# Kernel tuning notes

Measured on AMD Instinct MI355X. Metric: run time of the kernel, lower is better.

Reference implementation:

```python
import jax, jax.numpy as jnp
import numpy as np

S = 2048          # sequence length
E = 1024          # embedding_size
C = 16            # channels
ED = E // C       # per-channel dim e
VOCAB = 32000
EPS = 1e-8        # torch cosine_similarity eps


def setup_inputs() -> dict:
    key = jax.random.key(0)
    k0, k1, k2, k3, k4 = jax.random.split(key, 5)
    seqs = jax.random.randint(k0, (S,), 0, VOCAB - 1)  # avoid padding idx VOCAB-1
    emb = jax.random.uniform(k1, (VOCAB, E), minval=-0.05, maxval=0.05, dtype=jnp.float32)
    Wl = jax.random.normal(k2, (C, ED), dtype=jnp.float32) * 0.1
    Wr = jax.random.normal(k3, (C, ED), dtype=jnp.float32) * 0.1
    b = jax.random.normal(k4, (C, ED), dtype=jnp.float32) * 0.01
    return {"seqs": seqs, "emb": emb, "Wl": Wl, "Wr": Wr, "b": b}


def reference(seqs, emb, Wl, Wr, b):
    # Banyan.compose_words: greedy cosine-similarity adjacent-pair merge.
    # Fixed-size buffer + validity mask replaces torch's shrinking tensor so the
    # S-1 sequential merge steps run under a single lax.scan.
    x0 = emb[seqs]                      # [S, E]
    valid0 = jnp.ones((S,), dtype=bool)
    ar = jnp.arange(S)

    def comp(l, r):
        # channel-wise composition: view(2, c, e) -> parent [E]
        lc = l.reshape(C, ED)
        rc = r.reshape(C, ED)
        return jnp.tanh(lc * Wl + rc * Wr + b).reshape(E)

    def step(carry, _):
        x, valid = carry
        # next valid index for each position (suffix-min trick)
        idxs = jnp.where(valid, ar, S)
        nxt = jnp.flip(jax.lax.cummin(jnp.flip(jnp.append(idxs[1:], S))))
        pair_ok = valid & (nxt < S)
        xn = x[jnp.minimum(nxt, S - 1)]  # [S, E] right neighbor
        num = jnp.sum(x * xn, axis=-1)
        den = jnp.maximum(jnp.linalg.norm(x, axis=-1), EPS) * \
              jnp.maximum(jnp.linalg.norm(xn, axis=-1), EPS)
        cos = jnp.where(pair_ok, num / den, -jnp.inf)
        i = jnp.argmax(cos)              # left index of best adjacent pair
        j = nxt[i]                       # right index
        parent = comp(x[i], x[j])
        x = x.at[j].set(parent)          # parent overwrites right slot
        valid = valid.at[i].set(False)   # left slot removed
        return (x, valid), None

    (x, valid), _ = jax.lax.scan(step, (x0, valid0), None, length=S - 1)
    # exactly one valid slot remains -> root embedding [E]
    return jnp.sum(x * valid[:, None].astype(x.dtype), axis=0)
```

## Files before the change

kernel.cpp:

```cpp
#include <hip/hip_runtime.h>
#include <math.h>

#define SS 2048
#define EE 1024
#define EPSD 1e-8
#define EPSF 1e-8f
#define NTH 256
#define NW  4
#define NG  32
#define GS  64

#define DPP_XOR1 0xB1
#define DPP_XOR2 0x4E
#define DPP_HMIR 0x141
#define DPP_MIR  0x140

using f4 = float __attribute__((ext_vector_type(4)));
using f2 = float __attribute__((ext_vector_type(2)));

__device__ __forceinline__ void bar_lds() {
  asm volatile("s_waitcnt lgkmcnt(0)" ::: "memory");
  __builtin_amdgcn_s_barrier();
  __builtin_amdgcn_sched_barrier(0);
}

template <int CTRL>
__device__ __forceinline__ float mov_dpp_f32(float v) {
  union { float f; int i; } a; a.f = v;
  const int n = __builtin_amdgcn_mov_dpp(a.i, CTRL, 0xF, 0xF, true);
  union { int i; float f; } r; r.i = n;
  return r.f;
}

template <int CTRL>
__device__ __forceinline__ float dpp_addf(float v) { return v + mov_dpp_f32<CTRL>(v); }

template <int CTRL>
__device__ __forceinline__ void amax_dppf(float& v, int& ix) {
  const float ov = mov_dpp_f32<CTRL>(v);
  const int oi = __builtin_amdgcn_mov_dpp(ix, CTRL, 0xF, 0xF, true);
  if (ov > v || (ov == v && oi < ix)) { v = ov; ix = oi; }
}

__device__ __forceinline__ void foldmaxf(float& v, int& ix, float ov, int oi) {
  if (ov > v || (ov == v && oi < ix)) { v = ov; ix = oi; }
}

__device__ __forceinline__ float rsqrt1f(float x) {
  float y = __builtin_amdgcn_rsqf(x);
  y = y * fmaf(-0.5f * x * y, y, 1.5f);
  return y;
}

__device__ __forceinline__ float rcp1f(float x) {
  float y = __builtin_amdgcn_rcpf(x);
  y = y * fmaf(-x, y, 2.0f);
  return y;
}

__device__ __forceinline__ float tanh_f32(float z) {
  const float u = 0.5f * z;
  const float s = u * u;
  float P = fmaf(s, -929569.0f / 638512875.0f, 21844.0f / 6081075.0f);
  P = fmaf(s, P, -1382.0f / 155925.0f);
  P = fmaf(s, P, 62.0f / 2835.0f);
  P = fmaf(s, P, -17.0f / 315.0f);
  P = fmaf(s, P, 2.0f / 15.0f);
  P = fmaf(s, P, -1.0f / 3.0f);
  const float t = fmaf(u * s, P, u);
  const float den = fmaf(t, t, 1.0f);
  return (2.0f * t) * rcp1f(den);
}

__device__ __forceinline__ double wave_sum64(double v) {
#pragma unroll
  for (int off = 32; off > 0; off >>= 1) v += __shfl_down(v, off, 64);
  return v;
}

__global__ void banyan_init(const int* __restrict__ seqs, const float* __restrict__ emb,
                            float* __restrict__ x, double* __restrict__ norms) {
  __shared__ double sh[4];
  const int s = blockIdx.x;
  const int row = seqs[s];
  double acc = 0.0;
  for (int e = threadIdx.x; e < EE; e += 256) {
    const float v = emb[(size_t)row * EE + e];
    x[(size_t)s * EE + e] = v;
    acc += (double)v * (double)v;
  }
  acc = wave_sum64(acc);
  const int lane = threadIdx.x & 63;
  const int w = threadIdx.x >> 6;
  if (lane == 0) sh[w] = acc;
  __syncthreads();
  if (threadIdx.x == 0) norms[s] = sqrt(sh[0] + sh[1] + sh[2] + sh[3]);
}

__global__ void banyan_dots(const float* __restrict__ x, double* __restrict__ num) {
  __shared__ double sh[4];
  const int s = blockIdx.x;
  double acc = 0.0;
  for (int e = threadIdx.x; e < EE; e += 256) {
    acc += (double)x[(size_t)s * EE + e] * (double)x[(size_t)(s + 1) * EE + e];
  }
  acc = wave_sum64(acc);
  const int lane = threadIdx.x & 63;
  const int w = threadIdx.x >> 6;
  if (lane == 0) sh[w] = acc;
  __syncthreads();
  if (threadIdx.x == 0) num[s] = sh[0] + sh[1] + sh[2] + sh[3];
}

__global__ __launch_bounds__(NTH, 1) void banyan_main(
    float* __restrict__ x, const double* __restrict__ norms_in, const double* __restrict__ num_in,
    const float* __restrict__ Wl, const float* __restrict__ Wr, const float* __restrict__ Bb,
    float* __restrict__ out) {
  __shared__ float cosL[SS];
  __shared__ float rcpN[SS];
  __shared__ unsigned listL[SS];
  __shared__ int next2L[SS];
  __shared__ __align__(8) f2 gRec[NG];
  __shared__ float r3v[3][16];

  const int t = threadIdx.x;
  const int lane = t & 63;
  const int w = t >> 6;
  const int m16 = lane & 15;
  const float NEGINF = -__builtin_inff();

  for (int s = t; s < SS; s += NTH) {
    rcpN[s] = (float)(1.0 / fmax(norms_in[s], EPSD));
    const int nx = (s + 1 < SS) ? (s + 1) : -1;
    const int pv = s - 1;
    listL[s] = ((unsigned)nx & 0xFFFFu) | (((unsigned)pv & 0xFFFFu) << 16);
    next2L[s] = (s + 2 < SS) ? (s + 2) : -1;
  }
  __syncthreads();
  for (int s = t; s < SS; s += NTH) {
    cosL[s] = (s < SS - 1)
                  ? (float)((num_in[s] * (double)rcpN[s]) * (double)rcpN[s + 1])
                  : NEGINF;
  }
  __syncthreads();
  for (int m = 0; m < NG / NW; ++m) {
    const int g = w * (NG / NW) + m;
    float v = cosL[g * GS + lane];
    int ix = g * GS + lane;
#pragma unroll
    for (int off = 32; off > 0; off >>= 1) {
      const float ov = __shfl_down(v, off, 64);
      const int oi = __shfl_down(ix, off, 64);
      if (ov > v || (ov == v && oi < ix)) { v = ov; ix = oi; }
    }
    if (lane == 0) { f2 r; r.x = v; r.y = __int_as_float(ix); gRec[g] = r; }
  }
  __syncthreads();

  const int e0 = 4 * t;
  const f4 wl = *(const f4*)&Wl[e0];
  const f4 wr = *(const f4*)&Wr[e0];
  const f4 bv = *(const f4*)&Bb[e0];
  int head = 0;

  for (int step = 0; step < SS - 1; ++step) {
    const f2 rA = gRec[m16];
    const f2 rB = gRec[m16 + 16];
    float v = rA.x;
    int ix = __float_as_int(rA.y);
    foldmaxf(v, ix, rB.x, __float_as_int(rB.y));
    amax_dppf<DPP_XOR1>(v, ix);
    amax_dppf<DPP_XOR2>(v, ix);
    amax_dppf<DPP_HMIR>(v, ix);
    amax_dppf<DPP_MIR>(v, ix);
    const int i = __builtin_amdgcn_readfirstlane(ix);
    const f4 xi = *(const f4*)&x[(size_t)i * EE + e0];
    const unsigned pki = listL[i];
    const int nj_raw = next2L[i];
    const int j = __builtin_amdgcn_readfirstlane((int)(short)(pki & 0xFFFFu));
    const int p = __builtin_amdgcn_readfirstlane((int)(short)(pki >> 16));
    const int nj = __builtin_amdgcn_readfirstlane(nj_raw);
    if (p < 0) head = j;
    const int p2 = (p >= 0) ? p : i;
    const int n2 = (nj >= 0) ? nj : i;

    const f4 xj = *(const f4*)&x[(size_t)j * EE + e0];
    const f4 xp = *(const f4*)&x[(size_t)p2 * EE + e0];
    const f4 xn = *(const f4*)&x[(size_t)n2 * EE + e0];
    const float rcpP = rcpN[p2];
    const float rcpNN = rcpN[n2];
    const int gi_ = i >> 6;
    const int gp_ = (p >= 0) ? (p >> 6) : gi_;
    const int gj_ = j >> 6;
    const int grp = (w == 0) ? gi_ : (w == 1) ? gp_ : gj_;
    const int base = grp * GS + m16;

    float stv = NEGINF; int sti = 0;
    if (w < 3) {
      float cc0 = cosL[base];
      float cc1 = cosL[base + 16];
      float cc2 = cosL[base + 32];
      float cc3 = cosL[base + 48];
      const int pos0 = base, pos1 = base + 16, pos2 = base + 32, pos3 = base + 48;
      if (pos0 == i || pos0 == p || pos0 == j) cc0 = NEGINF;
      if (pos1 == i || pos1 == p || pos1 == j) cc1 = NEGINF;
      if (pos2 == i || pos2 == p || pos2 == j) cc2 = NEGINF;
      if (pos3 == i || pos3 == p || pos3 == j) cc3 = NEGINF;
      float cv = cc0; int gx = pos0;
      foldmaxf(cv, gx, cc1, pos1);
      foldmaxf(cv, gx, cc2, pos2);
      foldmaxf(cv, gx, cc3, pos3);
      amax_dppf<DPP_XOR1>(cv, gx);
      amax_dppf<DPP_XOR2>(cv, gx);
      amax_dppf<DPP_HMIR>(cv, gx);
      amax_dppf<DPP_MIR>(cv, gx);
      stv = cv; sti = gx;
    }

    const float q0 = tanh_f32(fmaf(xi.x, wl.x, fmaf(xj.x, wr.x, bv.x)));
    const float q1 = tanh_f32(fmaf(xi.y, wl.y, fmaf(xj.y, wr.y, bv.y)));
    const float q2 = tanh_f32(fmaf(xi.z, wl.z, fmaf(xj.z, wr.z, bv.z)));
    const float q3 = tanh_f32(fmaf(xi.w, wl.w, fmaf(xj.w, wr.w, bv.w)));

    float s0 = fmaf(q0, q0, fmaf(q1, q1, fmaf(q2, q2, q3 * q3)));
    float s1 = fmaf(xp.x, q0, fmaf(xp.y, q1, fmaf(xp.z, q2, xp.w * q3)));
    float s2 = fmaf(q0, xn.x, fmaf(q1, xn.y, fmaf(q2, xn.z, q3 * xn.w)));
    s1 = (p >= 0) ? s1 : 0.0f;
    s2 = (nj >= 0) ? s2 : 0.0f;
    s0 = dpp_addf<DPP_XOR1>(s0); s1 = dpp_addf<DPP_XOR1>(s1); s2 = dpp_addf<DPP_XOR1>(s2);
    s0 = dpp_addf<DPP_XOR2>(s0); s1 = dpp_addf<DPP_XOR2>(s1); s2 = dpp_addf<DPP_XOR2>(s2);
    s0 = dpp_addf<DPP_HMIR>(s0); s1 = dpp_addf<DPP_HMIR>(s1); s2 = dpp_addf<DPP_HMIR>(s2);
    s0 = dpp_addf<DPP_MIR>(s0);  s1 = dpp_addf<DPP_MIR>(s1);  s2 = dpp_addf<DPP_MIR>(s2);
    if (m16 == 0) {
      const int slot = w * 4 + (lane >> 4);
      r3v[0][slot] = s0; r3v[1][slot] = s1; r3v[2][slot] = s2;
    }
    bar_lds();

    {
      f4 st; st.x = q0; st.y = q1; st.z = q2; st.w = q3;
      *(f4*)&x[(size_t)j * EE + e0] = st;
    }
    float t0 = r3v[0][m16];
    float t1 = r3v[1][m16];
    float t2 = r3v[2][m16];
    t0 = dpp_addf<DPP_XOR1>(t0); t1 = dpp_addf<DPP_XOR1>(t1); t2 = dpp_addf<DPP_XOR1>(t2);
    t0 = dpp_addf<DPP_XOR2>(t0); t1 = dpp_addf<DPP_XOR2>(t1); t2 = dpp_addf<DPP_XOR2>(t2);
    t0 = dpp_addf<DPP_HMIR>(t0); t1 = dpp_addf<DPP_HMIR>(t1); t2 = dpp_addf<DPP_HMIR>(t2);
    t0 = dpp_addf<DPP_MIR>(t0);  t1 = dpp_addf<DPP_MIR>(t1);  t2 = dpp_addf<DPP_MIR>(t2);
    const float invnn = (t0 > EPSF * EPSF) ? rsqrt1f(t0) : 1e8f;
    const float cosP = (p >= 0) ? (t1 * rcpP) * invnn : NEGINF;
    const float cosJnew = (nj >= 0) ? (t2 * rcpNN) * invnn : NEGINF;
    if (w < 3) {
      float cv = stv; int gx = sti;
      if (p >= 0 && gp_ == grp) foldmaxf(cv, gx, cosP, p);
      if (gj_ == grp) foldmaxf(cv, gx, cosJnew, j);
      if (lane == 0) {
        f2 r; r.x = cv; r.y = __int_as_float(gx);
        gRec[grp] = r;
      }
    } else if (lane == 0) {
      cosL[i] = NEGINF;
      cosL[j] = cosJnew;
      rcpN[j] = invnn;
      listL[j] = ((unsigned)nj & 0xFFFFu) | (((unsigned)p & 0xFFFFu) << 16);
      if (p >= 0) {
        cosL[p] = cosP;
        const unsigned lp = listL[p];
        listL[p] = (lp & 0xFFFF0000u) | ((unsigned)j & 0xFFFFu);
        next2L[p] = nj;
        const int pp = (int)(short)(lp >> 16);
        if (pp >= 0) next2L[pp] = j;
      }
    }
    bar_lds();
  }

  {
    const f4 h = *(const f4*)&x[(size_t)head * EE + e0];
    *(f4*)&out[e0] = h;
  }
}

extern "C" void kernel_launch(void* const* d_in, const int* in_sizes, int n_in,
                              void* d_out, int out_size, void* d_ws, size_t ws_size,
                              hipStream_t stream) {
  const int* seqs = (const int*)d_in[0];
  const float* emb = (const float*)d_in[1];
  const float* Wl = (const float*)d_in[2];
  const float* Wr = (const float*)d_in[3];
  const float* Bb = (const float*)d_in[4];
  float* out = (float*)d_out;

  const size_t xbytesF = (size_t)SS * EE * sizeof(float);
  float* x = (float*)d_ws;
  double* norms = (double*)((char*)d_ws + xbytesF);
  double* num = norms + SS;
  hipLaunchKernelGGL(banyan_init, dim3(SS), dim3(256), 0, stream, seqs, emb, x, norms);
  hipLaunchKernelGGL(banyan_dots, dim3(SS - 1), dim3(256), 0, stream, x, num);
  hipLaunchKernelGGL(banyan_main, dim3(1), dim3(NTH), 0, stream,
                     x, norms, num, Wl, Wr, Bb, out);
}
```

Before: 2.571 ms.

## Compute next step's merge pair before the barrier to shorten the serial chain

Each step now also finds the next step's winning pair. Waves 0-2 publish their group maxima along with the neighbor-list entries, and wave 3 computes the best of the untouched groups. All of this is folded after the first barrier together with the updated cosP and cosJnew. The next i, j, p and nj are then available right after the second barrier, with no separate global argmax and no dependent LDS lookups at the top of the loop. The cost is extra LDS traffic and more complex bookkeeping, with a risk of stale neighbor data in edge cases such as the pp fixup.

```diff
diff --git a/kernel.cpp b/kernel.cpp
--- a/kernel.cpp
+++ b/kernel.cpp
@@ -17,6 +17,7 @@
 
 using f4 = float __attribute__((ext_vector_type(4)));
 using f2 = float __attribute__((ext_vector_type(2)));
+using i4 = int __attribute__((ext_vector_type(4)));
 
 __device__ __forceinline__ void bar_lds() {
   asm volatile("s_waitcnt lgkmcnt(0)" ::: "memory");
@@ -44,6 +45,11 @@
 
 __device__ __forceinline__ void foldmaxf(float& v, int& ix, float ov, int oi) {
   if (ov > v || (ov == v && oi < ix)) { v = ov; ix = oi; }
+}
+
+__device__ __forceinline__ void foldmax4(float& v, int& ix, int& pk, int& n2,
+                                         float ov, int oi, int opk, int on2) {
+  if (ov > v || (ov == v && oi < ix)) { v = ov; ix = oi; pk = opk; n2 = on2; }
 }
 
 __device__ __forceinline__ float rsqrt1f(float x) {
@@ -122,6 +128,8 @@
   __shared__ int next2L[SS];
   __shared__ __align__(8) f2 gRec[NG];
   __shared__ float r3v[3][16];
+  __shared__ __align__(16) int r4s[3][4];
+  __shared__ __align__(16) int r5s[4];
 
   const int t = threadIdx.x;
   const int lane = t & 63;
@@ -163,7 +171,8 @@
   const f4 bv = *(const f4*)&Bb[e0];
   int head = 0;
 
-  for (int step = 0; step < SS - 1; ++step) {
+  int i, j, p, nj, p2, n2, j2;
+  {
     const f2 rA = gRec[m16];
     const f2 rB = gRec[m16 + 16];
     float v = rA.x;
@@ -173,27 +182,34 @@
     amax_dppf<DPP_XOR2>(v, ix);
     amax_dppf<DPP_HMIR>(v, ix);
     amax_dppf<DPP_MIR>(v, ix);
-    const int i = __builtin_amdgcn_readfirstlane(ix);
+    i = __builtin_amdgcn_readfirstlane(ix);
+    const unsigned pki = listL[i];
+    j = (int)(short)(pki & 0xFFFFu);
+    p = (int)(short)(pki >> 16);
+    nj = next2L[i];
+    p2 = (p >= 0) ? p : i;
+    n2 = (nj >= 0) ? nj : i;
+    j2 = (j >= 0) ? j : i;
+  }
+
+  for (int step = 0; step < SS - 1; ++step) {
+    if (p < 0) head = j;
     const f4 xi = *(const f4*)&x[(size_t)i * EE + e0];
-    const unsigned pki = listL[i];
-    const int nj_raw = next2L[i];
-    const int j = __builtin_amdgcn_readfirstlane((int)(short)(pki & 0xFFFFu));
-    const int p = __builtin_amdgcn_readfirstlane((int)(short)(pki >> 16));
-    const int nj = __builtin_amdgcn_readfirstlane(nj_raw);
-    if (p < 0) head = j;
-    const int p2 = (p >= 0) ? p : i;
-    const int n2 = (nj >= 0) ? nj : i;
-
-    const f4 xj = *(const f4*)&x[(size_t)j * EE + e0];
+    const f4 xj = *(const f4*)&x[(size_t)j2 * EE + e0];
     const f4 xp = *(const f4*)&x[(size_t)p2 * EE + e0];
     const f4 xn = *(const f4*)&x[(size_t)n2 * EE + e0];
-    const float rcpP = rcpN[p2];
-    const float rcpNN = rcpN[n2];
+
     const int gi_ = i >> 6;
     const int gp_ = (p >= 0) ? (p >> 6) : gi_;
     const int gj_ = j >> 6;
     const int grp = (w == 0) ? gi_ : (w == 1) ? gp_ : gj_;
     const int base = grp * GS + m16;
+
+    const float rcpP = rcpN[p2];
+    const float rcpNN = rcpN[n2];
+    const unsigned lpp = listL[p2];
+    const int pp = (p >= 0) ? (int)(short)(lpp >> 16) : -1;
+    const int n2J = next2L[j2];
 
     float stv = NEGINF; int sti = 0;
     if (w < 3) {
@@ -215,6 +231,33 @@
       amax_dppf<DPP_HMIR>(cv, gx);
       amax_dppf<DPP_MIR>(cv, gx);
       stv = cv; sti = gx;
+      const int gxm = __builtin_amdgcn_readfirstlane(gx) & (SS - 1);
+      const unsigned lkU = listL[gxm];
+      const int n2U = next2L[gxm];
+      if (lane == 0) {
+        r4s[w][0] = __float_as_int(cv); r4s[w][1] = gx;
+        r4s[w][2] = (int)lkU; r4s[w][3] = n2U;
+      }
+    } else {
+      const f2 rA = gRec[m16];
+      const f2 rB = gRec[m16 + 16];
+      const bool mA = (m16 == gi_) | (m16 == gp_) | (m16 == gj_);
+      const int gB = m16 + 16;
+      const bool mB = (gB == gi_) | (gB == gp_) | (gB == gj_);
+      float sv = mA ? NEGINF : rA.x;
+      int si = __float_as_int(rA.y);
+      foldmaxf(sv, si, mB ? NEGINF : rB.x, __float_as_int(rB.y));
+      amax_dppf<DPP_XOR1>(sv, si);
+      amax_dppf<DPP_XOR2>(sv, si);
+      amax_dppf<DPP_HMIR>(sv, si);
+      amax_dppf<DPP_MIR>(sv, si);
+      const int siU = __builtin_amdgcn_readfirstlane(si) & (SS - 1);
+      const unsigned lkS = listL[siU];
+      const int n2S = next2L[siU];
+      if (lane == 0) {
+        r5s[0] = __float_as_int(sv); r5s[1] = si;
+        r5s[2] = (int)lkS; r5s[3] = n2S;
+      }
     }
 
     const float q0 = tanh_f32(fmaf(xi.x, wl.x, fmaf(xj.x, wr.x, bv.x)));
@@ -244,6 +287,10 @@
     float t0 = r3v[0][m16];
     float t1 = r3v[1][m16];
     float t2 = r3v[2][m16];
+    const i4 R0 = *(const i4*)&r4s[0][0];
+    const i4 R1 = *(const i4*)&r4s[1][0];
+    const i4 R2 = *(const i4*)&r4s[2][0];
+    const i4 R5 = *(const i4*)&r5s[0];
     t0 = dpp_addf<DPP_XOR1>(t0); t1 = dpp_addf<DPP_XOR1>(t1); t2 = dpp_addf<DPP_XOR1>(t2);
     t0 = dpp_addf<DPP_XOR2>(t0); t1 = dpp_addf<DPP_XOR2>(t1); t2 = dpp_addf<DPP_XOR2>(t2);
     t0 = dpp_addf<DPP_HMIR>(t0); t1 = dpp_addf<DPP_HMIR>(t1); t2 = dpp_addf<DPP_HMIR>(t2);
@@ -251,6 +298,22 @@
     const float invnn = (t0 > EPSF * EPSF) ? rsqrt1f(t0) : 1e8f;
     const float cosP = (p >= 0) ? (t1 * rcpP) * invnn : NEGINF;
     const float cosJnew = (nj >= 0) ? (t2 * rcpNN) * invnn : NEGINF;
+
+    float bvv = __int_as_float(R5.x); int bii = R5.y; int bpk = R5.z; int bn2 = R5.w;
+    foldmax4(bvv, bii, bpk, bn2, __int_as_float(R0.x), R0.y, R0.z, R0.w);
+    foldmax4(bvv, bii, bpk, bn2, __int_as_float(R1.x), R1.y, R1.z, R1.w);
+    foldmax4(bvv, bii, bpk, bn2, __int_as_float(R2.x), R2.y, R2.z, R2.w);
+    foldmax4(bvv, bii, bpk, bn2, cosP, p,
+             (int)(((unsigned)j & 0xFFFFu) | (((unsigned)pp & 0xFFFFu) << 16)), nj);
+    foldmax4(bvv, bii, bpk, bn2, cosJnew, j,
+             (int)(((unsigned)nj & 0xFFFFu) | (((unsigned)p & 0xFFFFu) << 16)), n2J);
+    if (bii != p && bii != j && bii == pp) bn2 = j;
+    const int iN = __builtin_amdgcn_readfirstlane(bii);
+    const unsigned bpkU = (unsigned)__builtin_amdgcn_readfirstlane(bpk);
+    const int njN = __builtin_amdgcn_readfirstlane(bn2);
+    const int jN = (int)(short)(bpkU & 0xFFFFu);
+    const int pN = (int)(short)(bpkU >> 16);
+
     if (w < 3) {
       float cv = stv; int gx = sti;
       if (p >= 0 && gp_ == grp) foldmaxf(cv, gx, cosP, p);
@@ -266,14 +329,16 @@
       listL[j] = ((unsigned)nj & 0xFFFFu) | (((unsigned)p & 0xFFFFu) << 16);
       if (p >= 0) {
         cosL[p] = cosP;
-        const unsigned lp = listL[p];
-        listL[p] = (lp & 0xFFFF0000u) | ((unsigned)j & 0xFFFFu);
+        listL[p] = (lpp & 0xFFFF0000u) | ((unsigned)j & 0xFFFFu);
         next2L[p] = nj;
-        const int pp = (int)(short)(lp >> 16);
         if (pp >= 0) next2L[pp] = j;
       }
     }
     bar_lds();
+    i = iN; j = jN; p = pN; nj = njN;
+    p2 = (p >= 0) ? p : i;
+    n2 = (nj >= 0) ? nj : i;
+    j2 = (j >= 0) ? j : i;
   }
 
   {
```

After: 2.786 ms. +8.3%, slower.

## Carry neighbor links with per-group argmax records to shorten the serial dependency chain

Applied to the files above, without the earlier changes.

Each group's max record now also stores the winner's packed prev/next link and next-next index, and these travel through the DPP argmax reduction. The per-step LDS lookups of listL/next2L for i are dropped from the critical path, so all four row loads from global memory can be issued right after the reduction. The price is extra DPP moves, extra LDS reads, and more complex bookkeeping to keep the cached links consistent, including a fix-up for the pp group's record.

```diff
diff --git a/kernel.cpp b/kernel.cpp
--- a/kernel.cpp
+++ b/kernel.cpp
@@ -42,8 +42,22 @@
   if (ov > v || (ov == v && oi < ix)) { v = ov; ix = oi; }
 }
 
+template <int CTRL>
+__device__ __forceinline__ void amax4_dppf(float& v, int& ix, int& pk, int& n2) {
+  const float ov = mov_dpp_f32<CTRL>(v);
+  const int oi = __builtin_amdgcn_mov_dpp(ix, CTRL, 0xF, 0xF, true);
+  const int op = __builtin_amdgcn_mov_dpp(pk, CTRL, 0xF, 0xF, true);
+  const int on = __builtin_amdgcn_mov_dpp(n2, CTRL, 0xF, 0xF, true);
+  if (ov > v || (ov == v && oi < ix)) { v = ov; ix = oi; pk = op; n2 = on; }
+}
+
 __device__ __forceinline__ void foldmaxf(float& v, int& ix, float ov, int oi) {
   if (ov > v || (ov == v && oi < ix)) { v = ov; ix = oi; }
+}
+
+__device__ __forceinline__ void foldmax4(float& v, int& ix, int& pk, int& n2,
+                                         float ov, int oi, int opk, int on2) {
+  if (ov > v || (ov == v && oi < ix)) { v = ov; ix = oi; pk = opk; n2 = on2; }
 }
 
 __device__ __forceinline__ float rsqrt1f(float x) {
@@ -121,6 +135,8 @@
   __shared__ unsigned listL[SS];
   __shared__ int next2L[SS];
   __shared__ __align__(8) f2 gRec[NG];
+  __shared__ int gLnkP[NG];
+  __shared__ int gLnkN[NG];
   __shared__ float r3v[3][16];
 
   const int t = threadIdx.x;
@@ -156,6 +172,12 @@
     if (lane == 0) { f2 r; r.x = v; r.y = __int_as_float(ix); gRec[g] = r; }
   }
   __syncthreads();
+  if (t < NG) {
+    const int ixg = __float_as_int(gRec[t].y) & (SS - 1);
+    gLnkP[t] = (int)listL[ixg];
+    gLnkN[t] = next2L[ixg];
+  }
+  __syncthreads();
 
   const int e0 = 4 * t;
   const f4 wl = *(const f4*)&Wl[e0];
@@ -166,29 +188,38 @@
   for (int step = 0; step < SS - 1; ++step) {
     const f2 rA = gRec[m16];
     const f2 rB = gRec[m16 + 16];
+    const int pkA = gLnkP[m16];
+    const int pkB = gLnkP[m16 + 16];
+    const int n2A = gLnkN[m16];
+    const int n2B = gLnkN[m16 + 16];
     float v = rA.x;
     int ix = __float_as_int(rA.y);
-    foldmaxf(v, ix, rB.x, __float_as_int(rB.y));
-    amax_dppf<DPP_XOR1>(v, ix);
-    amax_dppf<DPP_XOR2>(v, ix);
-    amax_dppf<DPP_HMIR>(v, ix);
-    amax_dppf<DPP_MIR>(v, ix);
+    int pkc = pkA;
+    int n2c_ = n2A;
+    foldmax4(v, ix, pkc, n2c_, rB.x, __float_as_int(rB.y), pkB, n2B);
+    amax4_dppf<DPP_XOR1>(v, ix, pkc, n2c_);
+    amax4_dppf<DPP_XOR2>(v, ix, pkc, n2c_);
+    amax4_dppf<DPP_HMIR>(v, ix, pkc, n2c_);
+    amax4_dppf<DPP_MIR>(v, ix, pkc, n2c_);
     const int i = __builtin_amdgcn_readfirstlane(ix);
-    const f4 xi = *(const f4*)&x[(size_t)i * EE + e0];
-    const unsigned pki = listL[i];
-    const int nj_raw = next2L[i];
-    const int j = __builtin_amdgcn_readfirstlane((int)(short)(pki & 0xFFFFu));
-    const int p = __builtin_amdgcn_readfirstlane((int)(short)(pki >> 16));
-    const int nj = __builtin_amdgcn_readfirstlane(nj_raw);
+    const unsigned pkU = (unsigned)__builtin_amdgcn_readfirstlane(pkc);
+    const int nj = __builtin_amdgcn_readfirstlane(n2c_);
+    const int j = (int)(short)(pkU & 0xFFFFu);
+    const int p = (int)(short)(pkU >> 16);
     if (p < 0) head = j;
     const int p2 = (p >= 0) ? p : i;
     const int n2 = (nj >= 0) ? nj : i;
 
+    const f4 xi = *(const f4*)&x[(size_t)i * EE + e0];
     const f4 xj = *(const f4*)&x[(size_t)j * EE + e0];
     const f4 xp = *(const f4*)&x[(size_t)p2 * EE + e0];
     const f4 xn = *(const f4*)&x[(size_t)n2 * EE + e0];
+
     const float rcpP = rcpN[p2];
     const float rcpNN = rcpN[n2];
+    const unsigned lpp = listL[p2];
+    const int pp = (p >= 0) ? (int)(short)(lpp >> 16) : -1;
+    const int n2J = next2L[(j >= 0) ? j : i];
     const int gi_ = i >> 6;
     const int gp_ = (p >= 0) ? (p >> 6) : gi_;
     const int gj_ = j >> 6;
@@ -196,6 +227,7 @@
     const int base = grp * GS + m16;
 
     float stv = NEGINF; int sti = 0;
+    unsigned lkW = 0u; int n2W = -1;
     if (w < 3) {
       float cc0 = cosL[base];
       float cc1 = cosL[base + 16];
@@ -215,6 +247,9 @@
       amax_dppf<DPP_HMIR>(cv, gx);
       amax_dppf<DPP_MIR>(cv, gx);
       stv = cv; sti = gx;
+      const int gxm = __builtin_amdgcn_readfirstlane(gx) & (SS - 1);
+      lkW = listL[gxm];
+      n2W = next2L[gxm];
     }
 
     const float q0 = tanh_f32(fmaf(xi.x, wl.x, fmaf(xj.x, wr.x, bv.x)));
@@ -251,13 +286,19 @@
     const float invnn = (t0 > EPSF * EPSF) ? rsqrt1f(t0) : 1e8f;
     const float cosP = (p >= 0) ? (t1 * rcpP) * invnn : NEGINF;
     const float cosJnew = (nj >= 0) ? (t2 * rcpNN) * invnn : NEGINF;
+    const int pk_p = (int)(((unsigned)j & 0xFFFFu) | (((unsigned)pp & 0xFFFFu) << 16));
+    const int pk_j = (int)(((unsigned)nj & 0xFFFFu) | (((unsigned)p & 0xFFFFu) << 16));
     if (w < 3) {
       float cv = stv; int gx = sti;
-      if (p >= 0 && gp_ == grp) foldmaxf(cv, gx, cosP, p);
-      if (gj_ == grp) foldmaxf(cv, gx, cosJnew, j);
+      int pkw = (int)lkW;
+      int n2w = (sti == pp) ? j : n2W;
+      if (p >= 0 && gp_ == grp) foldmax4(cv, gx, pkw, n2w, cosP, p, pk_p, nj);
+      if (gj_ == grp) foldmax4(cv, gx, pkw, n2w, cosJnew, j, pk_j, n2J);
       if (lane == 0) {
         f2 r; r.x = cv; r.y = __int_as_float(gx);
         gRec[grp] = r;
+        gLnkP[grp] = pkw;
+        gLnkN[grp] = n2w;
       }
     } else if (lane == 0) {
       cosL[i] = NEGINF;
@@ -266,11 +307,15 @@
       listL[j] = ((unsigned)nj & 0xFFFFu) | (((unsigned)p & 0xFFFFu) << 16);
       if (p >= 0) {
         cosL[p] = cosP;
-        const unsigned lp = listL[p];
-        listL[p] = (lp & 0xFFFF0000u) | ((unsigned)j & 0xFFFFu);
+        listL[p] = (lpp & 0xFFFF0000u) | ((unsigned)j & 0xFFFFu);
         next2L[p] = nj;
-        const int pp = (int)(short)(lp >> 16);
         if (pp >= 0) next2L[pp] = j;
+      }
+      if (pp >= 0) {
+        const int gpp = pp >> 6;
+        if (gpp != gi_ && gpp != gp_ && gpp != gj_) {
+          if (__float_as_int(gRec[gpp].y) == pp) gLnkN[gpp] = j;
+        }
       }
     }
     bar_lds();
```

After: 2.797 ms. 8.8% more time.
